# Kernel tuning notes

Measured on AMD Instinct MI355X. Metric: run time of the kernel, lower is better.

Reference implementation:

```python
import jax, jax.numpy as jnp
import numpy as np

NUM_PROP_LAYERS = 3


def _mlp3(x, w1, b1, w2, b2, w3, b3):
    h = jax.nn.relu(x @ w1 + b1)
    h = jax.nn.relu(h @ w2 + b2)
    return h @ w3 + b3


def setup_inputs() -> dict:
    key = jax.random.key(0)
    ks = jax.random.split(key, 20)
    B, N, D = 8, 4096, 128          # batch pairs, nodes per graph, node_state_dim
    E, ED = 524288, 64              # total edges, edge_feat_dim
    MH, MD, UH = 128, 128, 128      # message hidden, message dim, update hidden
    GH, GS = 256, 128               # graph hidden, graph state
    total = B * 2 * N

    def lin(k, fan_in, fan_out):
        return jax.random.normal(k, (fan_in, fan_out), jnp.float32) / np.sqrt(fan_in)

    return {
        "node_features": jax.random.normal(ks[0], (B, 2, N, D), jnp.float32),
        "edge_features": jax.random.normal(ks[1], (E, ED), jnp.float32),
        "edge_vertices": jax.random.randint(ks[2], (E, 2), 0, total, jnp.int64),
        # message encoder: (2D + ED) -> MH -> MH -> MD
        "msg_w1": lin(ks[3], 2 * D + ED, MH), "msg_b1": jnp.zeros((MH,), jnp.float32),
        "msg_w2": lin(ks[4], MH, MH),          "msg_b2": jnp.zeros((MH,), jnp.float32),
        "msg_w3": lin(ks[5], MH, MD),          "msg_b3": jnp.zeros((MD,), jnp.float32),
        # node update: (D + MD + D) -> UH -> UH -> D
        "upd_w1": lin(ks[6], 2 * D + MD, UH), "upd_b1": jnp.zeros((UH,), jnp.float32),
        "upd_w2": lin(ks[7], UH, UH),          "upd_b2": jnp.zeros((UH,), jnp.float32),
        "upd_w3": lin(ks[8], UH, D),           "upd_b3": jnp.zeros((D,), jnp.float32),
        # gate and aggregator
        "gate_w": lin(ks[9], D, D),   "gate_b": jnp.zeros((D,), jnp.float32),
        "agg_w1": lin(ks[10], D, GH), "agg_b1": jnp.zeros((GH,), jnp.float32),
        "agg_w2": lin(ks[11], GH, GS), "agg_b2": jnp.zeros((GS,), jnp.float32),
    }


def reference(node_features, edge_features, edge_vertices,
              msg_w1, msg_b1, msg_w2, msg_b2, msg_w3, msg_b3,
              upd_w1, upd_b1, upd_w2, upd_b2, upd_w3, upd_b3,
              gate_w, gate_b, agg_w1, agg_b1, agg_w2, agg_b2):
    B, two, N, D = node_features.shape
    total = B * two * N
    ns = node_features.reshape(total, D)
    src = edge_vertices[:, 0]
    dst = edge_vertices[:, 1]

    for _ in range(NUM_PROP_LAYERS):  # shared propagation-layer weights
        # gather endpoints, encode messages per edge
        msg_in = jnp.concatenate([ns[src], ns[dst], edge_features], axis=1)
        messages = _mlp3(msg_in, msg_w1, msg_b1, msg_w2, msg_b2, msg_w3, msg_b3)
        # scatter-add each message to both endpoints (torch scatter_add with
        # repeated messages + zero rows for every node == segment_sum below)
        summed = jax.ops.segment_sum(
            jnp.concatenate([messages, messages], axis=0),
            jnp.concatenate([src, dst], axis=0),
            num_segments=total)
        # cross-graph difference vectors per pair
        paired = ns.reshape(B, 2, N, D)
        att = jnp.concatenate([paired[:, 0] - paired[:, 1],
                               paired[:, 1] - paired[:, 0]], axis=1).reshape(total, D)
        upd_in = jnp.concatenate([ns, summed, att], axis=1)
        ns = _mlp3(upd_in, upd_w1, upd_b1, upd_w2, upd_b2, upd_w3, upd_b3)

    gates = jax.nn.sigmoid(ns @ gate_w + gate_b)
    ns = ns * gates
    graph_states = ns.reshape(B, 2, N, D).sum(axis=2)  # [B, 2, D]
    h = jax.nn.relu(graph_states @ agg_w1 + agg_b1)
    return h @ agg_w2 + agg_b2  # [B, 2, graph_state_dim]
```

## Files before the change

### kernel.cpp

```cpp
#include <hip/hip_runtime.h>
#include <math.h>

#define TOTAL  65536
#define NDIM   128
#define NEDGE  524288
#define EDIM   64

typedef __bf16 bf16x8 __attribute__((ext_vector_type(8)));
typedef float  f32x4  __attribute__((ext_vector_type(4)));
typedef unsigned int u32x4 __attribute__((ext_vector_type(4)));
typedef unsigned short u16x8 __attribute__((ext_vector_type(8)));

#define MFMA(a, b, c) __builtin_amdgcn_mfma_f32_16x16x32_bf16((a), (b), (c), 0, 0, 0)

static __device__ __forceinline__ float b2f(unsigned short u) {
    union { float f; unsigned int i; } v; v.i = ((unsigned int)u) << 16; return v.f;
}
static __device__ __forceinline__ unsigned short f2b(float f) {
    union { float f; unsigned int i; } v; v.f = f;
    unsigned int r = v.i + 0x7FFFu + ((v.i >> 16) & 1u);
    return (unsigned short)(r >> 16);
}
static __device__ __forceinline__ bf16x8 ldfrag(const unsigned short* p) {
    return __builtin_bit_cast(bf16x8, *(const u32x4*)p);
}
static __device__ __forceinline__ bf16x8 packf8(float4 a, float4 b) {
    u32x4 u;
    u[0] = (unsigned int)f2b(a.x) | ((unsigned int)f2b(a.y) << 16);
    u[1] = (unsigned int)f2b(a.z) | ((unsigned int)f2b(a.w) << 16);
    u[2] = (unsigned int)f2b(b.x) | ((unsigned int)f2b(b.y) << 16);
    u[3] = (unsigned int)f2b(b.z) | ((unsigned int)f2b(b.w) << 16);
    return __builtin_bit_cast(bf16x8, u);
}

__global__ __launch_bounds__(256) void cvt_kernel(
    const float* __restrict__ in, unsigned short* __restrict__ out, int n4)
{
    int i = blockIdx.x * 256 + threadIdx.x;
    if (i < n4) {
        float4 x = *(const float4*)&in[(size_t)i * 4];
        out[(size_t)i * 4 + 0] = f2b(x.x);
        out[(size_t)i * 4 + 1] = f2b(x.y);
        out[(size_t)i * 4 + 2] = f2b(x.z);
        out[(size_t)i * 4 + 3] = f2b(x.w);
    }
}

__global__ __launch_bounds__(256) void pkw_kernel(
    const float* __restrict__ src, unsigned short* __restrict__ dst, int KB)
{
    int idx = blockIdx.x * 256 + threadIdx.x;
    if (idx >= KB * 4096) return;
    const int j  = idx & 7;
    const int l  = (idx >> 3) & 63;
    const int nb = (idx >> 9) & 7;
    const int kb = idx >> 12;
    const int k   = kb * 32 + (l >> 4) * 8 + j;
    const int col = nb * 16 + (l & 15);
    dst[idx] = f2b(src[(size_t)k * 128 + col]);
}

__global__ __launch_bounds__(256) void pkef_kernel(
    const float* __restrict__ ef, unsigned short* __restrict__ out)
{
    const size_t idx = (size_t)blockIdx.x * 256 + threadIdx.x;
    const int j  = (int)(idx & 7);
    const int l  = (int)((idx >> 3) & 63);
    const int kb = (int)((idx >> 9) & 1);
    const int rt = (int)((idx >> 10) & 1);
    const int w  = (int)((idx >> 11) & 3);
    const size_t blk = idx >> 13;
    const size_t e = blk * 128 + w * 32 + rt * 16 + (l & 15);
    const int col = kb * 32 + (l >> 4) * 8 + j;
    out[idx] = f2b(ef[e * 64 + col]);
}

__global__ __launch_bounds__(256) void edge_mfma(
    const unsigned short* __restrict__ ns,
    const unsigned short* __restrict__ efp, const int* __restrict__ ev,
    const unsigned short* __restrict__ w1f,
    const unsigned short* __restrict__ w2f,
    const unsigned short* __restrict__ w3f,
    const float* __restrict__ b1, const float* __restrict__ b2,
    const float* __restrict__ b3, float* __restrict__ summed)
{
    __shared__ unsigned short s_h[128 * 128];
    __shared__ int s_src[128], s_dst[128];

    const int tid = threadIdx.x;
    const int w = tid >> 6, l = tid & 63;
    const int lr = l & 15, lg = l >> 4;
    const size_t eblk = (size_t)blockIdx.x * 128;

    {
        const int v = ev[eblk * 2 + tid];
        if (tid & 1) s_dst[tid >> 1] = v; else s_src[tid >> 1] = v;
    }
    __syncthreads();

    const int row0 = w * 32 + lr;
    const int row1 = row0 + 16;
    const int ms0 = s_src[row0], ms1 = s_src[row1];
    const int md0 = s_dst[row0], md1 = s_dst[row1];

    f32x4 acc0[8], acc1[8];
#pragma unroll
    for (int nb = 0; nb < 8; ++nb) {
        const float bv = b1[nb * 16 + lr];
        acc0[nb] = (f32x4){bv, bv, bv, bv};
        acc1[nb] = acc0[nb];
    }
#pragma unroll
    for (int kb = 0; kb < 4; ++kb) {
        const bf16x8 a0 = ldfrag(&ns[(size_t)ms0 * 128 + kb * 32 + lg * 8]);
        const bf16x8 a1 = ldfrag(&ns[(size_t)ms1 * 128 + kb * 32 + lg * 8]);
#pragma unroll
        for (int nb = 0; nb < 8; ++nb) {
            const bf16x8 bfr = ldfrag(&w1f[(size_t)((kb * 8 + nb) * 64 + l) * 8]);
            acc0[nb] = MFMA(a0, bfr, acc0[nb]);
            acc1[nb] = MFMA(a1, bfr, acc1[nb]);
        }
    }
#pragma unroll
    for (int kb = 0; kb < 4; ++kb) {
        const bf16x8 a0 = ldfrag(&ns[(size_t)md0 * 128 + kb * 32 + lg * 8]);
        const bf16x8 a1 = ldfrag(&ns[(size_t)md1 * 128 + kb * 32 + lg * 8]);
#pragma unroll
        for (int nb = 0; nb < 8; ++nb) {
            const bf16x8 bfr = ldfrag(&w1f[(size_t)(((kb + 4) * 8 + nb) * 64 + l) * 8]);
            acc0[nb] = MFMA(a0, bfr, acc0[nb]);
            acc1[nb] = MFMA(a1, bfr, acc1[nb]);
        }
    }
#pragma unroll
    for (int kb = 0; kb < 2; ++kb) {
        const size_t eb = (((size_t)blockIdx.x * 4 + w) * 4 + kb) * 512 + l * 8;
        const bf16x8 a0 = ldfrag(&efp[eb]);
        const bf16x8 a1 = ldfrag(&efp[eb + 1024]);
#pragma unroll
        for (int nb = 0; nb < 8; ++nb) {
            const bf16x8 bfr = ldfrag(&w1f[(size_t)(((kb + 8) * 8 + nb) * 64 + l) * 8]);
            acc0[nb] = MFMA(a0, bfr, acc0[nb]);
            acc1[nb] = MFMA(a1, bfr, acc1[nb]);
        }
    }
#pragma unroll
    for (int nb = 0; nb < 8; ++nb)
#pragma unroll
        for (int r = 0; r < 4; ++r) {
            const int ra = w * 32 + lg * 4 + r, rb = ra + 16;
            s_h[(ra * 128 + nb * 16 + lr) ^ ((ra & 7) << 3)] = f2b(fmaxf(acc0[nb][r], 0.f));
            s_h[(rb * 128 + nb * 16 + lr) ^ ((rb & 7) << 3)] = f2b(fmaxf(acc1[nb][r], 0.f));
        }

    const int sw0 = (row0 & 7) << 3, sw1 = (row1 & 7) << 3;
#pragma unroll
    for (int nb = 0; nb < 8; ++nb) {
        const float bv = b2[nb * 16 + lr];
        acc0[nb] = (f32x4){bv, bv, bv, bv};
        acc1[nb] = acc0[nb];
    }
#pragma unroll
    for (int kb = 0; kb < 4; ++kb) {
        const bf16x8 a0 = ldfrag(&s_h[(row0 * 128 + kb * 32 + lg * 8) ^ sw0]);
        const bf16x8 a1 = ldfrag(&s_h[(row1 * 128 + kb * 32 + lg * 8) ^ sw1]);
#pragma unroll
        for (int nb = 0; nb < 8; ++nb) {
            const bf16x8 bfr = ldfrag(&w2f[(size_t)((kb * 8 + nb) * 64 + l) * 8]);
            acc0[nb] = MFMA(a0, bfr, acc0[nb]);
            acc1[nb] = MFMA(a1, bfr, acc1[nb]);
        }
    }
#pragma unroll
    for (int nb = 0; nb < 8; ++nb)
#pragma unroll
        for (int r = 0; r < 4; ++r) {
            const int ra = w * 32 + lg * 4 + r, rb = ra + 16;
            s_h[(ra * 128 + nb * 16 + lr) ^ ((ra & 7) << 3)] = f2b(fmaxf(acc0[nb][r], 0.f));
            s_h[(rb * 128 + nb * 16 + lr) ^ ((rb & 7) << 3)] = f2b(fmaxf(acc1[nb][r], 0.f));
        }

#pragma unroll
    for (int nb = 0; nb < 8; ++nb) {
        const float bv = b3[nb * 16 + lr];
        acc0[nb] = (f32x4){bv, bv, bv, bv};
        acc1[nb] = acc0[nb];
    }
#pragma unroll
    for (int kb = 0; kb < 4; ++kb) {
        const bf16x8 a0 = ldfrag(&s_h[(row0 * 128 + kb * 32 + lg * 8) ^ sw0]);
        const bf16x8 a1 = ldfrag(&s_h[(row1 * 128 + kb * 32 + lg * 8) ^ sw1]);
#pragma unroll
        for (int nb = 0; nb < 8; ++nb) {
            const bf16x8 bfr = ldfrag(&w3f[(size_t)((kb * 8 + nb) * 64 + l) * 8]);
            acc0[nb] = MFMA(a0, bfr, acc0[nb]);
            acc1[nb] = MFMA(a1, bfr, acc1[nb]);
        }
    }

#pragma unroll
    for (int r = 0; r < 4; ++r) {
        const int ea = w * 32 + lg * 4 + r, eb2 = ea + 16;
        const size_t sa = (size_t)s_src[ea] * NDIM, da = (size_t)s_dst[ea] * NDIM;
        const size_t sb = (size_t)s_src[eb2] * NDIM, db = (size_t)s_dst[eb2] * NDIM;
#pragma unroll
        for (int nb = 0; nb < 8; ++nb) {
            const int col = nb * 16 + lr;
            const float v0 = acc0[nb][r], v1 = acc1[nb][r];
            atomicAdd(&summed[sa + col], v0);
            atomicAdd(&summed[da + col], v0);
            atomicAdd(&summed[sb + col], v1);
            atomicAdd(&summed[db + col], v1);
        }
    }
}

__global__ __launch_bounds__(256) void upd_mfma(
    const unsigned short* __restrict__ ns, const float* __restrict__ summed,
    const unsigned short* __restrict__ u1f,
    const unsigned short* __restrict__ u2f, const unsigned short* __restrict__ u3f,
    const float* __restrict__ ub1, const float* __restrict__ ub2,
    const float* __restrict__ ub3, unsigned short* __restrict__ out)
{
    __shared__ unsigned short s_h[64 * 128];

    const int tid = threadIdx.x;
    const int w = tid >> 6, l = tid & 63;
    const int lr = l & 15, lg = l >> 4;
    const int n0blk = blockIdx.x * 64;
    const int node = n0blk + w * 16 + lr;
    const int partner = node ^ 4096;

    bf16x8 nsf[4];
#pragma unroll
    for (int kb = 0; kb < 4; ++kb)
        nsf[kb] = ldfrag(&ns[(size_t)node * 128 + kb * 32 + lg * 8]);

    f32x4 acc[8];
#pragma unroll
    for (int nb = 0; nb < 8; ++nb) {
        const float bv = ub1[nb * 16 + lr];
        acc[nb] = (f32x4){bv, bv, bv, bv};
    }
#pragma unroll
    for (int kb = 0; kb < 4; ++kb) {
#pragma unroll
        for (int nb = 0; nb < 8; ++nb)
            acc[nb] = MFMA(nsf[kb], ldfrag(&u1f[(size_t)((kb * 8 + nb) * 64 + l) * 8]), acc[nb]);
    }
#pragma unroll
    for (int kb = 0; kb < 4; ++kb) {
        const float4 x0 = *(const float4*)&summed[(size_t)node * 128 + kb * 32 + lg * 8];
        const float4 x1 = *(const float4*)&summed[(size_t)node * 128 + kb * 32 + lg * 8 + 4];
        const bf16x8 af = packf8(x0, x1);
#pragma unroll
        for (int nb = 0; nb < 8; ++nb)
            acc[nb] = MFMA(af, ldfrag(&u1f[(size_t)(((kb + 4) * 8 + nb) * 64 + l) * 8]), acc[nb]);
    }
#pragma unroll
    for (int kb = 0; kb < 4; ++kb) {
        const u16x8 a = __builtin_bit_cast(u16x8, nsf[kb]);
        const u16x8 p = __builtin_bit_cast(u16x8, ldfrag(&ns[(size_t)partner * 128 + kb * 32 + lg * 8]));
        u16x8 o;
#pragma unroll
        for (int i = 0; i < 8; ++i) o[i] = f2b(b2f(a[i]) - b2f(p[i]));
        const bf16x8 af = __builtin_bit_cast(bf16x8, o);
#pragma unroll
        for (int nb = 0; nb < 8; ++nb)
            acc[nb] = MFMA(af, ldfrag(&u1f[(size_t)(((kb + 8) * 8 + nb) * 64 + l) * 8]), acc[nb]);
    }
#pragma unroll
    for (int nb = 0; nb < 8; ++nb)
#pragma unroll
        for (int r = 0; r < 4; ++r) {
            const int row = w * 16 + lg * 4 + r;
            s_h[(row * 128 + nb * 16 + lr) ^ ((row & 7) << 3)] = f2b(fmaxf(acc[nb][r], 0.f));
        }

    const int myrow = w * 16 + lr;
    const int asw = (myrow & 7) << 3;
#pragma unroll
    for (int nb = 0; nb < 8; ++nb) {
        const float bv = ub2[nb * 16 + lr];
        acc[nb] = (f32x4){bv, bv, bv, bv};
    }
#pragma unroll
    for (int kb = 0; kb < 4; ++kb) {
        const bf16x8 af = ldfrag(&s_h[(myrow * 128 + kb * 32 + lg * 8) ^ asw]);
#pragma unroll
        for (int nb = 0; nb < 8; ++nb)
            acc[nb] = MFMA(af, ldfrag(&u2f[(size_t)((kb * 8 + nb) * 64 + l) * 8]), acc[nb]);
    }
#pragma unroll
    for (int nb = 0; nb < 8; ++nb)
#pragma unroll
        for (int r = 0; r < 4; ++r) {
            const int row = w * 16 + lg * 4 + r;
            s_h[(row * 128 + nb * 16 + lr) ^ ((row & 7) << 3)] = f2b(fmaxf(acc[nb][r], 0.f));
        }

#pragma unroll
    for (int nb = 0; nb < 8; ++nb) {
        const float bv = ub3[nb * 16 + lr];
        acc[nb] = (f32x4){bv, bv, bv, bv};
    }
#pragma unroll
    for (int kb = 0; kb < 4; ++kb) {
        const bf16x8 af = ldfrag(&s_h[(myrow * 128 + kb * 32 + lg * 8) ^ asw]);
#pragma unroll
        for (int nb = 0; nb < 8; ++nb)
            acc[nb] = MFMA(af, ldfrag(&u3f[(size_t)((kb * 8 + nb) * 64 + l) * 8]), acc[nb]);
    }
#pragma unroll
    for (int nb = 0; nb < 8; ++nb)
#pragma unroll
        for (int r = 0; r < 4; ++r)
            out[(size_t)(n0blk + w * 16 + lg * 4 + r) * NDIM + nb * 16 + lr] = f2b(acc[nb][r]);
}

#define GPB 8
__global__ __launch_bounds__(128) void gate_kernel(
    const unsigned short* __restrict__ ns, const float* __restrict__ gw,
    const float* __restrict__ gb, float* __restrict__ gs)
{
    __shared__ float s_x[GPB][NDIM];
    const int j = threadIdx.x;
    const int n0 = blockIdx.x * GPB;
#pragma unroll
    for (int r = 0; r < GPB; ++r)
        s_x[r][j] = b2f(ns[(size_t)(n0 + r) * NDIM + j]);
    __syncthreads();

    float acc[GPB];
    const float bb = gb[j];
#pragma unroll
    for (int r = 0; r < GPB; ++r) acc[r] = bb;
    for (int i = 0; i < NDIM; i += 4) {
        const float w0 = gw[(i + 0) * NDIM + j];
        const float w1 = gw[(i + 1) * NDIM + j];
        const float wv2 = gw[(i + 2) * NDIM + j];
        const float wv3 = gw[(i + 3) * NDIM + j];
#pragma unroll
        for (int r = 0; r < GPB; ++r) {
            const float4 x = *(const float4*)&s_x[r][i];
            acc[r] = fmaf(x.x, w0, acc[r]);
            acc[r] = fmaf(x.y, w1, acc[r]);
            acc[r] = fmaf(x.z, wv2, acc[r]);
            acc[r] = fmaf(x.w, wv3, acc[r]);
        }
    }
    float part = 0.f;
#pragma unroll
    for (int r = 0; r < GPB; ++r) {
        const float g = 1.f / (1.f + expf(-acc[r]));
        part += s_x[r][j] * g;
    }
    atomicAdd(&gs[(n0 >> 12) * NDIM + j], part);
}

__global__ __launch_bounds__(256) void final_kernel(
    const float* __restrict__ gs,
    const float* __restrict__ aw1, const float* __restrict__ ab1,
    const float* __restrict__ aw2, const float* __restrict__ ab2,
    float* __restrict__ out)
{
    __shared__ float s_g[16 * 128];
    __shared__ float s_h[16 * 256];
    const int t = threadIdx.x;
    for (int k = t; k < 16 * 128; k += 256) s_g[k] = gs[k];
    __syncthreads();
    for (int r = 0; r < 16; ++r) {
        float a = ab1[t];
        for (int i = 0; i < 128; ++i)
            a = fmaf(s_g[r * 128 + i], aw1[i * 256 + t], a);
        s_h[r * 256 + t] = fmaxf(a, 0.f);
    }
    __syncthreads();
    for (int k = t; k < 16 * 128; k += 256) {
        const int r = k >> 7, j = k & 127;
        float a = ab2[j];
        for (int i = 0; i < 256; ++i)
            a = fmaf(s_h[r * 256 + i], aw2[i * 128 + j], a);
        out[k] = a;
    }
}

extern "C" void kernel_launch(void* const* d_in, const int* in_sizes, int n_in,
                              void* d_out, int out_size, void* d_ws, size_t ws_size,
                              hipStream_t stream)
{
    const float* nf      = (const float*)d_in[0];
    const float* ef      = (const float*)d_in[1];
    const int*   ev      = (const int*)d_in[2];
    const float* msg_w1  = (const float*)d_in[3];
    const float* msg_b1  = (const float*)d_in[4];
    const float* msg_w2  = (const float*)d_in[5];
    const float* msg_b2  = (const float*)d_in[6];
    const float* msg_w3  = (const float*)d_in[7];
    const float* msg_b3  = (const float*)d_in[8];
    const float* upd_w1  = (const float*)d_in[9];
    const float* upd_b1  = (const float*)d_in[10];
    const float* upd_w2  = (const float*)d_in[11];
    const float* upd_b2  = (const float*)d_in[12];
    const float* upd_w3  = (const float*)d_in[13];
    const float* upd_b3  = (const float*)d_in[14];
    const float* gate_w  = (const float*)d_in[15];
    const float* gate_b  = (const float*)d_in[16];
    const float* agg_w1  = (const float*)d_in[17];
    const float* agg_b1  = (const float*)d_in[18];
    const float* agg_w2  = (const float*)d_in[19];
    const float* agg_b2  = (const float*)d_in[20];

    const size_t NS = (size_t)TOTAL * NDIM;
    unsigned short* ns0 = (unsigned short*)d_ws;
    unsigned short* nsA = ns0 + NS;
    unsigned short* nsB = nsA + NS;
    float* summed = (float*)(nsB + NS);
    float* gs     = summed + NS;
    unsigned short* w1f = (unsigned short*)(gs + 16 * NDIM);
    unsigned short* w2f = w1f + 10 * 4096;
    unsigned short* w3f = w2f + 4 * 4096;
    unsigned short* u1f = w3f + 4 * 4096;
    unsigned short* u2f = u1f + 12 * 4096;
    unsigned short* u3f = u2f + 4 * 4096;
    unsigned short* efp = u3f + 4 * 4096;

    cvt_kernel<<<(int)(NS / 4 + 255) / 256, 256, 0, stream>>>(nf, ns0, (int)(NS / 4));
    pkw_kernel<<<10 * 16, 256, 0, stream>>>(msg_w1, w1f, 10);
    pkw_kernel<<< 4 * 16, 256, 0, stream>>>(msg_w2, w2f, 4);
    pkw_kernel<<< 4 * 16, 256, 0, stream>>>(msg_w3, w3f, 4);
    pkw_kernel<<<12 * 16, 256, 0, stream>>>(upd_w1, u1f, 12);
    pkw_kernel<<< 4 * 16, 256, 0, stream>>>(upd_w2, u2f, 4);
    pkw_kernel<<< 4 * 16, 256, 0, stream>>>(upd_w3, u3f, 4);
    pkef_kernel<<<(int)((size_t)NEDGE * EDIM / 256), 256, 0, stream>>>(ef, efp);

    const unsigned short* curs[3] = { ns0, nsA, nsB };
    unsigned short* nxts[3]       = { nsA, nsB, nsA };
    for (int lyr = 0; lyr < 3; ++lyr) {
        hipMemsetAsync(summed, 0, NS * sizeof(float), stream);
        edge_mfma<<<NEDGE / 128, 256, 0, stream>>>(curs[lyr], efp, ev, w1f, w2f, w3f,
                                                   msg_b1, msg_b2, msg_b3, summed);
        upd_mfma<<<TOTAL / 64, 256, 0, stream>>>(curs[lyr], summed, u1f, u2f, u3f,
                                                 upd_b1, upd_b2, upd_b3, nxts[lyr]);
    }
    hipMemsetAsync(gs, 0, (size_t)16 * NDIM * sizeof(float), stream);
    gate_kernel<<<TOTAL / GPB, 128, 0, stream>>>(nsA, gate_w, gate_b, gs);
    final_kernel<<<1, 256, 0, stream>>>(gs, agg_w1, agg_b1, agg_w2, agg_b2,
                                        (float*)d_out);
}
```

Measured before the change: 2.121 ms.

## Replace atomic scatter-add with CSR build and per-node gather of bf16 messages

Instead of each edge doing fp32 atomicAdds into a summed buffer for both endpoints, the code builds a CSR (histogram, scan, fill) once per call. Each layer now writes bf16 messages per edge and sums them per node in a gather kernel, with the sum handed to the update kernel in bf16. This removes heavy atomic contention and the per-layer memset. In exchange it adds an extra message buffer write and read, a single-block scan, and gather load imbalance, and it lowers summation precision to bf16 storage. There is also a fallback that reads raw fp32 edge features when the workspace is too small.

Result: faster. 1.800 ms (-15.1%).

```diff
diff --git a/kernel.cpp b/kernel.cpp
--- a/kernel.cpp
+++ b/kernel.cpp
@@ -75,14 +75,58 @@
     out[idx] = f2b(ef[e * 64 + col]);
 }
 
+__global__ __launch_bounds__(256) void hist_kernel(
+    const int* __restrict__ ev, unsigned int* __restrict__ cnt)
+{
+    const int t = blockIdx.x * 256 + threadIdx.x;
+    atomicAdd(&cnt[ev[t]], 1u);
+}
+
+__global__ __launch_bounds__(1024) void scan_kernel(
+    const unsigned int* __restrict__ cnt, unsigned int* __restrict__ rowptr,
+    unsigned int* __restrict__ cursor)
+{
+    __shared__ unsigned int part[1024];
+    const int t = threadIdx.x;
+    unsigned int s = 0;
+    for (int j = 0; j < 64; ++j) s += cnt[t * 64 + j];
+    part[t] = s;
+    __syncthreads();
+    for (int off = 1; off < 1024; off <<= 1) {
+        unsigned int v = (t >= off) ? part[t - off] : 0u;
+        __syncthreads();
+        part[t] += v;
+        __syncthreads();
+    }
+    unsigned int run = (t == 0) ? 0u : part[t - 1];
+    for (int j = 0; j < 64; ++j) {
+        rowptr[t * 64 + j] = run;
+        cursor[t * 64 + j] = run;
+        run += cnt[t * 64 + j];
+    }
+    if (t == 1023) rowptr[65536] = part[1023];
+}
+
+__global__ __launch_bounds__(256) void fill_kernel(
+    const int* __restrict__ ev, unsigned int* __restrict__ cursor,
+    unsigned int* __restrict__ eidx)
+{
+    const int e = blockIdx.x * 256 + threadIdx.x;
+    const int s = ev[2 * e], d = ev[2 * e + 1];
+    unsigned int p = atomicAdd(&cursor[s], 1u); eidx[p] = (unsigned int)e;
+    unsigned int q = atomicAdd(&cursor[d], 1u); eidx[q] = (unsigned int)e;
+}
+
+template<int EFP>
 __global__ __launch_bounds__(256) void edge_mfma(
     const unsigned short* __restrict__ ns,
-    const unsigned short* __restrict__ efp, const int* __restrict__ ev,
+    const unsigned short* __restrict__ efp, const float* __restrict__ ef,
+    const int* __restrict__ ev,
     const unsigned short* __restrict__ w1f,
     const unsigned short* __restrict__ w2f,
     const unsigned short* __restrict__ w3f,
     const float* __restrict__ b1, const float* __restrict__ b2,
-    const float* __restrict__ b3, float* __restrict__ summed)
+    const float* __restrict__ b3, unsigned short* __restrict__ msg)
 {
     __shared__ unsigned short s_h[128 * 128];
     __shared__ int s_src[128], s_dst[128];
@@ -134,9 +178,18 @@
     }
 #pragma unroll
     for (int kb = 0; kb < 2; ++kb) {
-        const size_t eb = (((size_t)blockIdx.x * 4 + w) * 4 + kb) * 512 + l * 8;
-        const bf16x8 a0 = ldfrag(&efp[eb]);
-        const bf16x8 a1 = ldfrag(&efp[eb + 1024]);
+        bf16x8 a0, a1;
+        if (EFP) {
+            const size_t eb = (((size_t)blockIdx.x * 4 + w) * 4 + kb) * 512 + l * 8;
+            a0 = ldfrag(&efp[eb]);
+            a1 = ldfrag(&efp[eb + 1024]);
+        } else {
+            const size_t er0 = eblk + row0, er1 = eblk + row1;
+            a0 = packf8(*(const float4*)&ef[er0 * EDIM + kb * 32 + lg * 8],
+                        *(const float4*)&ef[er0 * EDIM + kb * 32 + lg * 8 + 4]);
+            a1 = packf8(*(const float4*)&ef[er1 * EDIM + kb * 32 + lg * 8],
+                        *(const float4*)&ef[er1 * EDIM + kb * 32 + lg * 8 + 4]);
+        }
 #pragma unroll
         for (int nb = 0; nb < 8; ++nb) {
             const bf16x8 bfr = ldfrag(&w1f[(size_t)(((kb + 8) * 8 + nb) * 64 + l) * 8]);
@@ -197,26 +250,46 @@
             acc1[nb] = MFMA(a1, bfr, acc1[nb]);
         }
     }
-
-#pragma unroll
-    for (int r = 0; r < 4; ++r) {
-        const int ea = w * 32 + lg * 4 + r, eb2 = ea + 16;
-        const size_t sa = (size_t)s_src[ea] * NDIM, da = (size_t)s_dst[ea] * NDIM;
-        const size_t sb = (size_t)s_src[eb2] * NDIM, db = (size_t)s_dst[eb2] * NDIM;
-#pragma unroll
-        for (int nb = 0; nb < 8; ++nb) {
-            const int col = nb * 16 + lr;
-            const float v0 = acc0[nb][r], v1 = acc1[nb][r];
-            atomicAdd(&summed[sa + col], v0);
-            atomicAdd(&summed[da + col], v0);
-            atomicAdd(&summed[sb + col], v1);
-            atomicAdd(&summed[db + col], v1);
-        }
+#pragma unroll
+    for (int nb = 0; nb < 8; ++nb)
+#pragma unroll
+        for (int r = 0; r < 4; ++r) {
+            const int ra = w * 32 + lg * 4 + r, rb = ra + 16;
+            s_h[(ra * 128 + nb * 16 + lr) ^ ((ra & 7) << 3)] = f2b(acc0[nb][r]);
+            s_h[(rb * 128 + nb * 16 + lr) ^ ((rb & 7) << 3)] = f2b(acc1[nb][r]);
+        }
+#pragma unroll
+    for (int it = 0; it < 8; ++it) {
+        const int row = w * 32 + it * 4 + lg;
+        const int sw = (row & 7) << 3;
+        const u32x4 v = *(const u32x4*)&s_h[(row * 128 + lr * 8) ^ sw];
+        *(u32x4*)&msg[(eblk + row) * 128 + lr * 8] = v;
+    }
+}
+
+__global__ __launch_bounds__(256) void gather_kernel(
+    const unsigned short* __restrict__ msg, const unsigned int* __restrict__ rowptr,
+    const unsigned int* __restrict__ eidx, unsigned short* __restrict__ sumb)
+{
+    const int w = threadIdx.x >> 6, l = threadIdx.x & 63;
+#pragma unroll
+    for (int i = 0; i < 2; ++i) {
+        const int n = blockIdx.x * 8 + w * 2 + i;
+        const unsigned int beg = rowptr[n], end = rowptr[n + 1];
+        float s0 = 0.f, s1 = 0.f;
+        for (unsigned int p = beg; p < end; ++p) {
+            const unsigned int e = eidx[p];
+            const unsigned int v = *(const unsigned int*)&msg[(size_t)e * 128 + l * 2];
+            s0 += b2f((unsigned short)(v & 0xffffu));
+            s1 += b2f((unsigned short)(v >> 16));
+        }
+        const unsigned int o = (unsigned int)f2b(s0) | ((unsigned int)f2b(s1) << 16);
+        *(unsigned int*)&sumb[(size_t)n * 128 + l * 2] = o;
     }
 }
 
 __global__ __launch_bounds__(256) void upd_mfma(
-    const unsigned short* __restrict__ ns, const float* __restrict__ summed,
+    const unsigned short* __restrict__ ns, const unsigned short* __restrict__ sumb,
     const unsigned short* __restrict__ u1f,
     const unsigned short* __restrict__ u2f, const unsigned short* __restrict__ u3f,
     const float* __restrict__ ub1, const float* __restrict__ ub2,
@@ -250,9 +323,7 @@
     }
 #pragma unroll
     for (int kb = 0; kb < 4; ++kb) {
-        const float4 x0 = *(const float4*)&summed[(size_t)node * 128 + kb * 32 + lg * 8];
-        const float4 x1 = *(const float4*)&summed[(size_t)node * 128 + kb * 32 + lg * 8 + 4];
-        const bf16x8 af = packf8(x0, x1);
+        const bf16x8 af = ldfrag(&sumb[(size_t)node * 128 + kb * 32 + lg * 8]);
 #pragma unroll
         for (int nb = 0; nb < 8; ++nb)
             acc[nb] = MFMA(af, ldfrag(&u1f[(size_t)(((kb + 4) * 8 + nb) * 64 + l) * 8]), acc[nb]);
@@ -412,18 +483,27 @@
     const float* agg_b2  = (const float*)d_in[20];
 
     const size_t NS = (size_t)TOTAL * NDIM;
-    unsigned short* ns0 = (unsigned short*)d_ws;
-    unsigned short* nsA = ns0 + NS;
-    unsigned short* nsB = nsA + NS;
-    float* summed = (float*)(nsB + NS);
-    float* gs     = summed + NS;
-    unsigned short* w1f = (unsigned short*)(gs + 16 * NDIM);
-    unsigned short* w2f = w1f + 10 * 4096;
-    unsigned short* w3f = w2f + 4 * 4096;
-    unsigned short* u1f = w3f + 4 * 4096;
-    unsigned short* u2f = u1f + 12 * 4096;
-    unsigned short* u3f = u2f + 4 * 4096;
-    unsigned short* efp = u3f + 4 * 4096;
+    unsigned short* p = (unsigned short*)d_ws;
+    unsigned short* ns0 = p;            p += NS;
+    unsigned short* nsA = p;            p += NS;
+    unsigned short* nsB = p;            p += NS;
+    unsigned short* sumb = p;           p += NS;
+    unsigned short* w1f = p;            p += 10 * 4096;
+    unsigned short* w2f = p;            p += 4 * 4096;
+    unsigned short* w3f = p;            p += 4 * 4096;
+    unsigned short* u1f = p;            p += 12 * 4096;
+    unsigned short* u2f = p;            p += 4 * 4096;
+    unsigned short* u3f = p;            p += 4 * 4096;
+    float* gs = (float*)p;              p += 2 * 16 * NDIM;
+    unsigned int* cnt    = (unsigned int*)p;  p += 2 * 65536;
+    unsigned int* cursor = (unsigned int*)p;  p += 2 * 65536;
+    unsigned int* rowptr = (unsigned int*)p;  p += 2 * 65540;
+    unsigned int* eidx   = (unsigned int*)p;  p += 2 * 2 * NEDGE;
+    unsigned short* msg  = p;           p += (size_t)NEDGE * 128;
+    unsigned short* efp  = p;           p += (size_t)NEDGE * EDIM;
+
+    const size_t need_full = (size_t)(p - (unsigned short*)d_ws) * 2;
+    const bool use_efp = ws_size >= need_full;
 
     cvt_kernel<<<(int)(NS / 4 + 255) / 256, 256, 0, stream>>>(nf, ns0, (int)(NS / 4));
     pkw_kernel<<<10 * 16, 256, 0, stream>>>(msg_w1, w1f, 10);
@@ -432,19 +512,29 @@
     pkw_kernel<<<12 * 16, 256, 0, stream>>>(upd_w1, u1f, 12);
     pkw_kernel<<< 4 * 16, 256, 0, stream>>>(upd_w2, u2f, 4);
     pkw_kernel<<< 4 * 16, 256, 0, stream>>>(upd_w3, u3f, 4);
-    pkef_kernel<<<(int)((size_t)NEDGE * EDIM / 256), 256, 0, stream>>>(ef, efp);
+    if (use_efp)
+        pkef_kernel<<<(int)((size_t)NEDGE * EDIM / 256), 256, 0, stream>>>(ef, efp);
+
+    hipMemsetAsync(cnt, 0, 65536 * sizeof(unsigned int), stream);
+    hist_kernel<<<2 * NEDGE / 256, 256, 0, stream>>>(ev, cnt);
+    scan_kernel<<<1, 1024, 0, stream>>>(cnt, rowptr, cursor);
+    fill_kernel<<<NEDGE / 256, 256, 0, stream>>>(ev, cursor, eidx);
 
     const unsigned short* curs[3] = { ns0, nsA, nsB };
-    unsigned short* nxts[3]       = { nsA, nsB, nsA };
+    unsigned short* nxts[3]       = { nsA, nsB, ns0 };
     for (int lyr = 0; lyr < 3; ++lyr) {
-        hipMemsetAsync(summed, 0, NS * sizeof(float), stream);
-        edge_mfma<<<NEDGE / 128, 256, 0, stream>>>(curs[lyr], efp, ev, w1f, w2f, w3f,
-                                                   msg_b1, msg_b2, msg_b3, summed);
-        upd_mfma<<<TOTAL / 64, 256, 0, stream>>>(curs[lyr], summed, u1f, u2f, u3f,
+        if (use_efp)
+            edge_mfma<1><<<NEDGE / 128, 256, 0, stream>>>(curs[lyr], efp, ef, ev,
+                w1f, w2f, w3f, msg_b1, msg_b2, msg_b3, msg);
+        else
+            edge_mfma<0><<<NEDGE / 128, 256, 0, stream>>>(curs[lyr], efp, ef, ev,
+                w1f, w2f, w3f, msg_b1, msg_b2, msg_b3, msg);
+        gather_kernel<<<TOTAL / 8, 256, 0, stream>>>(msg, rowptr, eidx, sumb);
+        upd_mfma<<<TOTAL / 64, 256, 0, stream>>>(curs[lyr], sumb, u1f, u2f, u3f,
                                                  upd_b1, upd_b2, upd_b3, nxts[lyr]);
     }
     hipMemsetAsync(gs, 0, (size_t)16 * NDIM * sizeof(float), stream);
-    gate_kernel<<<TOTAL / GPB, 128, 0, stream>>>(nsA, gate_w, gate_b, gs);
+    gate_kernel<<<TOTAL / GPB, 128, 0, stream>>>(ns0, gate_w, gate_b, gs);
     final_kernel<<<1, 256, 0, stream>>>(gs, agg_w1, agg_b1, agg_w2, agg_b2,
                                         (float*)d_out);
 }
```
